# Kernel tuning notes

Measured on AMD Instinct MI355X. Metric: run time of the kernel, lower is better.

Reference implementation:

```python
import jax, jax.numpy as jnp
import numpy as np
import math

B, S, HID = 2, 2048, 1024
NH = 16
HD = HID // NH  # 64
CHUNK = 128  # min(128, S) from the module


def setup_inputs() -> dict:
    key = jax.random.key(0)
    ks = jax.random.split(key, 8)
    scale = 1.0 / math.sqrt(HID)
    return {
        "hidden_states": jax.random.normal(ks[0], (B, S, HID), jnp.float32),
        "attention_mask": jnp.zeros((B, S, S), jnp.float32),
        "Wq": jax.random.normal(ks[1], (HID, HID), jnp.float32) * scale,
        "bq": jnp.zeros((HID,), jnp.float32),
        "Wk": jax.random.normal(ks[2], (HID, HID), jnp.float32) * scale,
        "bk": jnp.zeros((HID,), jnp.float32),
        "Wv": jax.random.normal(ks[3], (HID, HID), jnp.float32) * scale,
        "bv": jnp.zeros((HID,), jnp.float32),
        "head_weights": jnp.ones((NH,), jnp.float32),
    }


def _split_heads(x):
    # [B,S,HID] -> [B,NH,S,HD]
    b, s, _ = x.shape
    return x.reshape(b, s, NH, HD).transpose(0, 2, 1, 3)


def reference(hidden_states, attention_mask, Wq, bq, Wk, bk, Wv, bv, head_weights):
    # nn.Linear: y = x @ W.T + b
    q = _split_heads(hidden_states @ Wq.T + bq)  # [B,NH,S,HD]
    k = _split_heads(hidden_states @ Wk.T + bk)
    v = _split_heads(hidden_states @ Wv.T + bv)

    scores = jnp.einsum("bhqd,bhkd->bhqk", q, k) / math.sqrt(HD)
    scores = scores + attention_mask[:, None, :, :]  # additive mask broadcast over heads
    probs = jax.nn.softmax(scores, axis=-1)
    # dropout p=0.0 -> identity; post-softmax head-weight scaling (head_pruning)
    probs = probs * head_weights[None, :, None, None]
    ctx = jnp.einsum("bhqk,bhkd->bhqd", probs, v)  # [B,NH,S,HD]
    context_layer = ctx.transpose(0, 2, 1, 3).reshape(B, S, HID)

    # module returns the probs of the LAST query chunk of the python loop
    last_start = ((S + CHUNK - 1) // CHUNK - 1) * CHUNK
    output_attention_probs = probs[:, :, last_start:S, :]  # [B,NH,128,S]
    return context_layer, output_attention_probs
```

## Files before the change

### kernel.cpp

```cpp
#include <hip/hip_runtime.h>

typedef unsigned short u16;
typedef __attribute__((ext_vector_type(8))) short bf16x8;
typedef __attribute__((ext_vector_type(4))) float f32x4;

#define B_   2
#define S_   2048
#define HID_ 1024
#define NH_  16
#define HD_  64
#define SCALE_ 0.125f

__device__ __forceinline__ u16 f2bf(float f) {
    union { float f; unsigned int i; } v; v.f = f;
    unsigned int r = v.i + 0x7fffu + ((v.i >> 16) & 1u);
    return (u16)(r >> 16);
}
__device__ __forceinline__ bf16x8 ld8(const u16* p) {
    return *reinterpret_cast<const bf16x8*>(p);
}
__device__ __forceinline__ void gll16(const u16* g, const u16* l) {
    __builtin_amdgcn_global_load_lds(
        (const __attribute__((address_space(1))) unsigned int*)g,
        (__attribute__((address_space(3))) unsigned int*)l, 16, 0, 0);
}

__global__ __launch_bounds__(256) void convert_bf16(
    const float* __restrict__ X, const float* __restrict__ W0,
    const float* __restrict__ W1, const float* __restrict__ W2,
    u16* __restrict__ Xb, u16* __restrict__ Wb)
{
    const size_t s = (size_t)blockIdx.x * 256 + threadIdx.x;
    const float* src; u16* dst; size_t off;
    if (s < 524288) { src = X; dst = Xb; off = s * 8; }
    else {
        const size_t t = s - 524288;
        const int w = (int)(t >> 17);
        off = (t & 131071) * 8;
        src = w == 0 ? W0 : w == 1 ? W1 : W2;
        dst = Wb + (size_t)w * 1048576;
    }
    f32x4 a = *(const f32x4*)(src + off);
    f32x4 b = *(const f32x4*)(src + off + 4);
    bf16x8 r;
    #pragma unroll
    for (int e = 0; e < 4; e++) { r[e] = (short)f2bf(a[e]); r[4 + e] = (short)f2bf(b[e]); }
    *(bf16x8*)(dst + off) = r;
}

__global__ __launch_bounds__(256) void mask_scan(
    const unsigned* __restrict__ m, unsigned* __restrict__ flag)
{
    const size_t i = ((size_t)blockIdx.x * 256 + threadIdx.x) * 8;
    const uint4* p = (const uint4*)(m + i);
    uint4 a = p[0], b = p[1];
    const unsigned M = 0x7fffffffu;
    unsigned v = (a.x & M) | (a.y & M) | (a.z & M) | (a.w & M)
               | (b.x & M) | (b.y & M) | (b.z & M) | (b.w & M);
    if (v) atomicOr(flag, 1u);
}

#define BK_ 32

__global__ __launch_bounds__(256) void qkv_mfma(
    const u16* __restrict__ Xb, const u16* __restrict__ Wb,
    const float* __restrict__ bq, const float* __restrict__ bk,
    const float* __restrict__ bv,
    u16* __restrict__ Q, u16* __restrict__ K, u16* __restrict__ V)
{
    __shared__ __align__(16) u16 As[128 * BK_];
    __shared__ __align__(16) u16 Bs[128 * BK_];

    const int tid  = threadIdx.x;
    const int wave = tid >> 6;
    const int lane = tid & 63;
    const int l16  = lane & 15;
    const int quad = lane >> 4;
    const int wr   = wave >> 1, wc = wave & 1;

    const int i0 = blockIdx.x * 128;
    const int j0 = blockIdx.y * 128;

    const int grow = (wave * 64 + lane) >> 2;
    const int gcol = (lane & 3) * 8;
    const u16* ldsA0 = As + wave * 512;
    const u16* ldsA1 = As + 2048 + wave * 512;
    const u16* ldsB0 = Bs + wave * 512;
    const u16* ldsB1 = Bs + 2048 + wave * 512;

    f32x4 acc[4][4] = {};

    for (int k0 = 0; k0 < HID_; k0 += BK_) {
        __syncthreads();
        gll16(Xb + (size_t)(i0 + grow) * HID_ + k0 + gcol, ldsA0);
        gll16(Xb + (size_t)(i0 + 64 + grow) * HID_ + k0 + gcol, ldsA1);
        gll16(Wb + (size_t)(j0 + grow) * HID_ + k0 + gcol, ldsB0);
        gll16(Wb + (size_t)(j0 + 64 + grow) * HID_ + k0 + gcol, ldsB1);
        __syncthreads();

        bf16x8 af[4], bfr[4];
        #pragma unroll
        for (int mt = 0; mt < 4; mt++)
            af[mt] = ld8(&As[(wr * 64 + mt * 16 + l16) * BK_ + quad * 8]);
        #pragma unroll
        for (int nt = 0; nt < 4; nt++)
            bfr[nt] = ld8(&Bs[(wc * 64 + nt * 16 + l16) * BK_ + quad * 8]);
        #pragma unroll
        for (int mt = 0; mt < 4; mt++)
            #pragma unroll
            for (int nt = 0; nt < 4; nt++)
                acc[mt][nt] = __builtin_amdgcn_mfma_f32_16x16x32_bf16(af[mt], bfr[nt], acc[mt][nt], 0, 0, 0);
    }

    const int which = j0 >> 10;
    const float* bias = which == 0 ? bq : which == 1 ? bk : bv;
    u16* Y            = which == 0 ? Q  : which == 1 ? K  : V;

    u16* bb = (wave < 2) ? (As + wave * 2048) : (Bs + (wave - 2) * 2048);

    #pragma unroll
    for (int p = 0; p < 2; p++) {
        __syncthreads();
        #pragma unroll
        for (int t2 = 0; t2 < 2; t2++) {
            const int nt = 2 * p + t2;
            const int j  = j0 + wc * 64 + nt * 16 + l16;
            const int jj = j & 1023;
            const float bv_ = bias[jj];
            #pragma unroll
            for (int mt = 0; mt < 4; mt++)
                #pragma unroll
                for (int r = 0; r < 4; r++) {
                    const int row = mt * 16 + quad * 4 + r;
                    const int col = t2 * 16 + l16;
                    const u16 val = f2bf(acc[mt][nt][r] + bv_);
                    if (which == 2)
                        bb[col * 64 + (row ^ ((col & 7) << 3))] = val;
                    else
                        bb[row * 32 + (col ^ ((row & 0xC) << 1))] = val;
                }
        }
        __syncthreads();
        #pragma unroll
        for (int k = 0; k < 4; k++) {
            const int c = lane + 64 * k;
            if (which == 2) {
                const int col  = c >> 3;
                const int row0 = (c & 7) * 8;
                bf16x8 v = ld8(&bb[col * 64 + (row0 ^ ((col & 7) << 3))]);
                const int j  = j0 + wc * 64 + p * 32 + col;
                const int jj = j & 1023;
                const int h = jj >> 6, d = jj & 63;
                const int i = i0 + wr * 64 + row0;
                const int b = i >> 11, s = i & (S_ - 1);
                *(bf16x8*)&Y[((size_t)(b * NH_ + h) * HD_ + d) * S_ + s] = v;
            } else {
                const int row  = c >> 2;
                const int col0 = (c & 3) * 8;
                bf16x8 v = ld8(&bb[row * 32 + (col0 ^ ((row & 0xC) << 1))]);
                const int j  = j0 + wc * 64 + p * 32 + col0;
                const int jj = j & 1023;
                const int h = jj >> 6, d = jj & 63;
                const int i = i0 + wr * 64 + row;
                const int b = i >> 11, s = i & (S_ - 1);
                *(bf16x8*)&Y[(((size_t)(b * NH_ + h) * S_ + s) * HD_) + d] = v;
            }
        }
    }
}

__global__ __launch_bounds__(256) void attn(
    const u16* __restrict__ Q, const u16* __restrict__ K, const u16* __restrict__ Vt,
    const float* __restrict__ mask, const float* __restrict__ hw,
    const unsigned* __restrict__ mflag,
    float* __restrict__ ctx, float* __restrict__ probs_out, float* __restrict__ ml)
{
    __shared__ __align__(16) u16 Ks[2][64 * 64];
    __shared__ __align__(16) u16 Vs[2][64 * 64];
    __shared__ __align__(16) u16 Pl[4][16 * 64];

    const int usemask = (mflag[0] != 0);

    const int tid  = threadIdx.x;
    const int wave = tid >> 6;
    const int lane = tid & 63;
    const int l16  = lane & 15;
    const int quad = lane >> 4;
    const int x7   = l16 & 7;

    const int lin = blockIdx.x + 32 * (blockIdx.y + 16 * blockIdx.z);
    const int xcd = lin & 7, jj = lin >> 3;
    const int qb  = jj & 31;
    const int hb  = xcd * 4 + (jj >> 5);
    const int h   = hb & 15, b = hb >> 4;
    const int bh  = b * NH_ + h;

    const u16* Qh  = Q  + (size_t)bh * S_ * HD_;
    const u16* Kh  = K  + (size_t)bh * S_ * HD_;
    const u16* Vth = Vt + (size_t)bh * HD_ * S_;
    const float* Mb = mask + (size_t)b * S_ * S_;

    const int q0 = qb * 64 + wave * 16;

    bf16x8 qf0 = ld8(Qh + (size_t)(q0 + l16) * HD_ + quad * 8);
    bf16x8 qf1 = ld8(Qh + (size_t)(q0 + l16) * HD_ + 32 + quad * 8);

    f32x4 oacc[4] = {};
    float l_part[4] = {0.f, 0.f, 0.f, 0.f};

    const int srow = tid >> 3;
    const int sch  = tid & 7;
    const int ssw  = (sch ^ (srow & 7)) * 8;
    const int sL   = srow * 64 + ssw;

    {
        bf16x8 k0 = ld8(Kh + (size_t)srow * HD_ + sch * 8);
        bf16x8 k1 = ld8(Kh + (size_t)(srow + 32) * HD_ + sch * 8);
        bf16x8 v0 = ld8(Vth + (size_t)srow * S_ + sch * 8);
        bf16x8 v1 = ld8(Vth + (size_t)(srow + 32) * S_ + sch * 8);
        *(bf16x8*)&Ks[0][sL] = k0; *(bf16x8*)&Ks[0][sL + 2048] = k1;
        *(bf16x8*)&Vs[0][sL] = v0; *(bf16x8*)&Vs[0][sL + 2048] = v1;
    }
    __syncthreads();

    for (int t = 0; t < 32; ++t) {
        const int cur = t & 1;
        const int kt  = t * 64;
        const u16* Kb = Ks[cur];
        const u16* Vb = Vs[cur];

        bf16x8 kr0, kr1, vr0, vr1;
        if (t < 31) {
            const u16* Kg = Kh + (size_t)(kt + 64) * HD_;
            kr0 = ld8(Kg + (size_t)srow * HD_ + sch * 8);
            kr1 = ld8(Kg + (size_t)(srow + 32) * HD_ + sch * 8);
            vr0 = ld8(Vth + (size_t)srow * S_ + kt + 64 + sch * 8);
            vr1 = ld8(Vth + (size_t)(srow + 32) * S_ + kt + 64 + sch * 8);
        }

        f32x4 sacc[4] = {};
        #pragma unroll
        for (int nb = 0; nb < 4; nb++) {
            const int base = (nb * 16 + l16) * 64;
            bf16x8 k0 = ld8(&Kb[base + ((quad ^ x7) * 8)]);
            bf16x8 k1 = ld8(&Kb[base + (((quad + 4) ^ x7) * 8)]);
            sacc[nb] = __builtin_amdgcn_mfma_f32_16x16x32_bf16(qf0, k0, sacc[nb], 0, 0, 0);
            sacc[nb] = __builtin_amdgcn_mfma_f32_16x16x32_bf16(qf1, k1, sacc[nb], 0, 0, 0);
        }
        float sc[4][4];
        if (usemask) {
            #pragma unroll
            for (int nb = 0; nb < 4; nb++)
                #pragma unroll
                for (int r = 0; r < 4; r++) {
                    const int qrow = q0 + quad * 4 + r;
                    const int key  = kt + nb * 16 + l16;
                    sc[nb][r] = sacc[nb][r] * SCALE_ + Mb[(size_t)qrow * S_ + key];
                }
        } else {
            #pragma unroll
            for (int nb = 0; nb < 4; nb++)
                #pragma unroll
                for (int r = 0; r < 4; r++) sc[nb][r] = sacc[nb][r] * SCALE_;
        }

        if (qb >= 30) {
            #pragma unroll
            for (int nb = 0; nb < 4; nb++)
                #pragma unroll
                for (int r = 0; r < 4; r++) {
                    const int qrow = q0 + quad * 4 + r;
                    const int key  = kt + nb * 16 + l16;
                    probs_out[((size_t)bh * 128 + (qrow - 1920)) * S_ + key] = sc[nb][r];
                }
        }

        u16 pb[4][4];
        #pragma unroll
        for (int nb = 0; nb < 4; nb++)
            #pragma unroll
            for (int r = 0; r < 4; r++) {
                float p = __expf(fminf(sc[nb][r], 80.f));
                l_part[r] += p;
                pb[nb][r] = f2bf(p);
            }

        #pragma unroll
        for (int nb = 0; nb < 4; nb++)
            #pragma unroll
            for (int r = 0; r < 4; r++) {
                const int row = quad * 4 + r;
                const int boff = (nb * 32 + l16 * 2) ^ ((row & 7) << 4);
                *(u16*)((char*)&Pl[wave][0] + row * 128 + boff) = pb[nb][r];
            }

        #pragma unroll
        for (int kb = 0; kb < 2; kb++) {
            const int c = kb * 4 + quad;
            bf16x8 pf = ld8(&Pl[wave][l16 * 64 + ((c ^ x7) * 8)]);
            #pragma unroll
            for (int db = 0; db < 4; db++) {
                bf16x8 vf = ld8(&Vb[(db * 16 + l16) * 64 + ((c ^ x7) * 8)]);
                oacc[db] = __builtin_amdgcn_mfma_f32_16x16x32_bf16(pf, vf, oacc[db], 0, 0, 0);
            }
        }

        if (t < 31) {
            u16* Kd = Ks[cur ^ 1]; u16* Vd = Vs[cur ^ 1];
            *(bf16x8*)&Kd[sL] = kr0; *(bf16x8*)&Kd[sL + 2048] = kr1;
            *(bf16x8*)&Vd[sL] = vr0; *(bf16x8*)&Vd[sL + 2048] = vr1;
        }
        __syncthreads();
    }

    float l_i[4];
    #pragma unroll
    for (int r = 0; r < 4; r++) {
        float s = l_part[r];
        #pragma unroll
        for (int off = 1; off < 16; off <<= 1) s += __shfl_xor(s, off);
        l_i[r] = s;
    }

    const float hwf = hw[h];
    float invl[4];
    #pragma unroll
    for (int r = 0; r < 4; r++) invl[r] = hwf / l_i[r];

    #pragma unroll
    for (int db = 0; db < 4; db++)
        #pragma unroll
        for (int r = 0; r < 4; r++) {
            const int qrow = q0 + quad * 4 + r;
            ctx[((size_t)(b * S_ + qrow)) * HID_ + h * HD_ + db * 16 + l16] =
                oacc[db][r] * invl[r];
        }

    if (qb >= 30 && l16 == 0) {
        #pragma unroll
        for (int r = 0; r < 4; r++) {
            const int qrow = q0 + quad * 4 + r;
            ml[bh * 128 + (qrow - 1920)] = l_i[r];
        }
    }
}

__global__ __launch_bounds__(256) void probs_finish(
    float* __restrict__ probs, const float* __restrict__ ml,
    const float* __restrict__ hw)
{
    const size_t i = ((size_t)blockIdx.x * 256 + threadIdx.x) * 4;
    const int row = (int)(i >> 11);
    const int h   = (row >> 7) & 15;
    const float s = hw[h] / ml[row];
    float4 v = *(float4*)(probs + i);
    v.x = __expf(fminf(v.x, 80.f)) * s;
    v.y = __expf(fminf(v.y, 80.f)) * s;
    v.z = __expf(fminf(v.z, 80.f)) * s;
    v.w = __expf(fminf(v.w, 80.f)) * s;
    *(float4*)(probs + i) = v;
}

extern "C" void kernel_launch(void* const* d_in, const int* in_sizes, int n_in,
                              void* d_out, int out_size, void* d_ws, size_t ws_size,
                              hipStream_t stream)
{
    const void* X = 0; const void* mask = 0; const void* hw = 0;
    const void* Wm[3] = {0, 0, 0}; const void* bm[3] = {0, 0, 0};
    int wi = 0, bi = 0;
    for (int i = 0; i < n_in; i++) {
        switch (in_sizes[i]) {
            case 4194304: X = d_in[i]; break;
            case 8388608: mask = d_in[i]; break;
            case 1048576: if (wi < 3) Wm[wi++] = d_in[i]; break;
            case 1024:    if (bi < 3) bm[bi++] = d_in[i]; break;
            case 16:      hw = d_in[i]; break;
            default: break;
        }
    }
    if (!X || !mask || wi != 3 || bi != 3 || !hw) {
        X = d_in[0]; mask = d_in[1];
        Wm[0] = d_in[2]; bm[0] = d_in[3];
        Wm[1] = d_in[4]; bm[1] = d_in[5];
        Wm[2] = d_in[6]; bm[2] = d_in[7];
        hw = d_in[8];
    }

    u16* Q  = (u16*)d_ws;
    u16* Kw = Q + 4194304ull;
    u16* Vw = Kw + 4194304ull;
    u16* Xb = Vw + 4194304ull;
    u16* Wb = Xb + 4194304ull;
    unsigned* flag = (unsigned*)(Wb + 3145728ull);
    float* ml = (float*)(flag + 64);

    float* ctx   = (float*)d_out;
    float* probs = ctx + (size_t)B_ * S_ * HID_;

    hipMemsetAsync(flag, 0, 4, stream);
    mask_scan<<<4096, 256, 0, stream>>>((const unsigned*)mask, flag);
    convert_bf16<<<3584, 256, 0, stream>>>(
        (const float*)X, (const float*)Wm[0], (const float*)Wm[1], (const float*)Wm[2],
        Xb, Wb);

    qkv_mfma<<<dim3(32, 24), dim3(256), 0, stream>>>(
        Xb, Wb, (const float*)bm[0], (const float*)bm[1], (const float*)bm[2],
        Q, Kw, Vw);

    attn<<<dim3(32, 16, 2), dim3(256), 0, stream>>>(
        Q, Kw, Vw, (const float*)mask, (const float*)hw, flag, ctx, probs, ml);

    probs_finish<<<8192, 256, 0, stream>>>(probs, ml, (const float*)hw);
}
```

Before: 256.6 us.

## Double-buffer QKV GEMM, fuse probs normalization into attention, add setprio and packed bf16 cvt

The QKV GEMM now double-buffers its LDS tiles and prefetches the next K slice while the current one feeds the MFMAs, leaving one barrier per iteration. In the attention kernel, exp is computed once and unnormalized probabilities are written for the last query chunk. Those rows are then rescaled in place at the end of the kernel, which removes the separate probs_finish launch and the ml buffer. It also adds s_setprio around the MFMA sections and uses packed v_cvt_pk_bf16_f32 conversion for P. The in-kernel rescale rereads each row from global memory after stores made by other lanes in the same wave, so correctness depends on that visibility holding.

```diff
diff --git a/kernel.cpp b/kernel.cpp
--- a/kernel.cpp
+++ b/kernel.cpp
@@ -18,6 +18,11 @@
 }
 __device__ __forceinline__ bf16x8 ld8(const u16* p) {
     return *reinterpret_cast<const bf16x8*>(p);
+}
+__device__ __forceinline__ unsigned cvtpk(float lo, float hi) {
+    unsigned r;
+    asm("v_cvt_pk_bf16_f32 %0, %1, %2" : "=v"(r) : "v"(lo), "v"(hi));
+    return r;
 }
 __device__ __forceinline__ void gll16(const u16* g, const u16* l) {
     __builtin_amdgcn_global_load_lds(
@@ -68,8 +73,8 @@
     const float* __restrict__ bv,
     u16* __restrict__ Q, u16* __restrict__ K, u16* __restrict__ V)
 {
-    __shared__ __align__(16) u16 As[128 * BK_];
-    __shared__ __align__(16) u16 Bs[128 * BK_];
+    __shared__ __align__(16) u16 As[2][128 * BK_];
+    __shared__ __align__(16) u16 Bs[2][128 * BK_];
 
     const int tid  = threadIdx.x;
     const int wave = tid >> 6;
@@ -81,42 +86,46 @@
     const int i0 = blockIdx.x * 128;
     const int j0 = blockIdx.y * 128;
 
-    const int grow = (wave * 64 + lane) >> 2;
+    const int grow = tid >> 2;
     const int gcol = (lane & 3) * 8;
-    const u16* ldsA0 = As + wave * 512;
-    const u16* ldsA1 = As + 2048 + wave * 512;
-    const u16* ldsB0 = Bs + wave * 512;
-    const u16* ldsB1 = Bs + 2048 + wave * 512;
 
     f32x4 acc[4][4] = {};
 
-    for (int k0 = 0; k0 < HID_; k0 += BK_) {
-        __syncthreads();
-        gll16(Xb + (size_t)(i0 + grow) * HID_ + k0 + gcol, ldsA0);
-        gll16(Xb + (size_t)(i0 + 64 + grow) * HID_ + k0 + gcol, ldsA1);
-        gll16(Wb + (size_t)(j0 + grow) * HID_ + k0 + gcol, ldsB0);
-        gll16(Wb + (size_t)(j0 + 64 + grow) * HID_ + k0 + gcol, ldsB1);
-        __syncthreads();
+    auto stage = [&](int bf, int k0) {
+        gll16(Xb + (size_t)(i0 + grow) * HID_ + k0 + gcol, &As[bf][wave * 512]);
+        gll16(Xb + (size_t)(i0 + 64 + grow) * HID_ + k0 + gcol, &As[bf][2048 + wave * 512]);
+        gll16(Wb + (size_t)(j0 + grow) * HID_ + k0 + gcol, &Bs[bf][wave * 512]);
+        gll16(Wb + (size_t)(j0 + 64 + grow) * HID_ + k0 + gcol, &Bs[bf][2048 + wave * 512]);
+    };
+
+    stage(0, 0);
+    __syncthreads();
+
+    for (int t = 0; t < 32; t++) {
+        const int cur = t & 1;
+        if (t < 31) stage(cur ^ 1, (t + 1) * BK_);
 
         bf16x8 af[4], bfr[4];
         #pragma unroll
         for (int mt = 0; mt < 4; mt++)
-            af[mt] = ld8(&As[(wr * 64 + mt * 16 + l16) * BK_ + quad * 8]);
+            af[mt] = ld8(&As[cur][(wr * 64 + mt * 16 + l16) * BK_ + quad * 8]);
         #pragma unroll
         for (int nt = 0; nt < 4; nt++)
-            bfr[nt] = ld8(&Bs[(wc * 64 + nt * 16 + l16) * BK_ + quad * 8]);
+            bfr[nt] = ld8(&Bs[cur][(wc * 64 + nt * 16 + l16) * BK_ + quad * 8]);
         #pragma unroll
         for (int mt = 0; mt < 4; mt++)
             #pragma unroll
             for (int nt = 0; nt < 4; nt++)
                 acc[mt][nt] = __builtin_amdgcn_mfma_f32_16x16x32_bf16(af[mt], bfr[nt], acc[mt][nt], 0, 0, 0);
+
+        __syncthreads();
     }
 
     const int which = j0 >> 10;
     const float* bias = which == 0 ? bq : which == 1 ? bk : bv;
     u16* Y            = which == 0 ? Q  : which == 1 ? K  : V;
 
-    u16* bb = (wave < 2) ? (As + wave * 2048) : (Bs + (wave - 2) * 2048);
+    u16* bb = (wave < 2) ? &As[0][wave * 2048] : &Bs[0][(wave - 2) * 2048];
 
     #pragma unroll
     for (int p = 0; p < 2; p++) {
@@ -173,7 +182,7 @@
     const u16* __restrict__ Q, const u16* __restrict__ K, const u16* __restrict__ Vt,
     const float* __restrict__ mask, const float* __restrict__ hw,
     const unsigned* __restrict__ mflag,
-    float* __restrict__ ctx, float* __restrict__ probs_out, float* __restrict__ ml)
+    float* __restrict__ ctx, float* __restrict__ probs_out)
 {
     __shared__ __align__(16) u16 Ks[2][64 * 64];
     __shared__ __align__(16) u16 Vs[2][64 * 64];
@@ -239,6 +248,7 @@
         }
 
         f32x4 sacc[4] = {};
+        __builtin_amdgcn_s_setprio(1);
         #pragma unroll
         for (int nb = 0; nb < 4; nb++) {
             const int base = (nb * 16 + l16) * 64;
@@ -247,7 +257,9 @@
             sacc[nb] = __builtin_amdgcn_mfma_f32_16x16x32_bf16(qf0, k0, sacc[nb], 0, 0, 0);
             sacc[nb] = __builtin_amdgcn_mfma_f32_16x16x32_bf16(qf1, k1, sacc[nb], 0, 0, 0);
         }
-        float sc[4][4];
+        __builtin_amdgcn_s_setprio(0);
+
+        float p[4][4];
         if (usemask) {
             #pragma unroll
             for (int nb = 0; nb < 4; nb++)
@@ -255,13 +267,18 @@
                 for (int r = 0; r < 4; r++) {
                     const int qrow = q0 + quad * 4 + r;
                     const int key  = kt + nb * 16 + l16;
-                    sc[nb][r] = sacc[nb][r] * SCALE_ + Mb[(size_t)qrow * S_ + key];
+                    float s = sacc[nb][r] * SCALE_ + Mb[(size_t)qrow * S_ + key];
+                    p[nb][r] = __expf(fminf(s, 80.f));
+                    l_part[r] += p[nb][r];
                 }
         } else {
             #pragma unroll
             for (int nb = 0; nb < 4; nb++)
                 #pragma unroll
-                for (int r = 0; r < 4; r++) sc[nb][r] = sacc[nb][r] * SCALE_;
+                for (int r = 0; r < 4; r++) {
+                    p[nb][r] = __expf(fminf(sacc[nb][r] * SCALE_, 80.f));
+                    l_part[r] += p[nb][r];
+                }
         }
 
         if (qb >= 30) {
@@ -271,29 +288,26 @@
                 for (int r = 0; r < 4; r++) {
                     const int qrow = q0 + quad * 4 + r;
                     const int key  = kt + nb * 16 + l16;
-                    probs_out[((size_t)bh * 128 + (qrow - 1920)) * S_ + key] = sc[nb][r];
+                    probs_out[((size_t)bh * 128 + (qrow - 1920)) * S_ + key] = p[nb][r];
                 }
         }
 
-        u16 pb[4][4];
-        #pragma unroll
-        for (int nb = 0; nb < 4; nb++)
-            #pragma unroll
-            for (int r = 0; r < 4; r++) {
-                float p = __expf(fminf(sc[nb][r], 80.f));
-                l_part[r] += p;
-                pb[nb][r] = f2bf(p);
+        {
+            char* pbase = (char*)&Pl[wave][0];
+            const int r0 = quad * 4;
+            #pragma unroll
+            for (int nb = 0; nb < 4; nb++) {
+                const unsigned w01 = cvtpk(p[nb][0], p[nb][1]);
+                const unsigned w23 = cvtpk(p[nb][2], p[nb][3]);
+                const int c0 = nb * 32 + l16 * 2;
+                *(u16*)(pbase + (r0 + 0) * 128 + (c0 ^ (((r0 + 0) & 7) << 4))) = (u16)w01;
+                *(u16*)(pbase + (r0 + 1) * 128 + (c0 ^ (((r0 + 1) & 7) << 4))) = (u16)(w01 >> 16);
+                *(u16*)(pbase + (r0 + 2) * 128 + (c0 ^ (((r0 + 2) & 7) << 4))) = (u16)w23;
+                *(u16*)(pbase + (r0 + 3) * 128 + (c0 ^ (((r0 + 3) & 7) << 4))) = (u16)(w23 >> 16);
             }
-
-        #pragma unroll
-        for (int nb = 0; nb < 4; nb++)
-            #pragma unroll
-            for (int r = 0; r < 4; r++) {
-                const int row = quad * 4 + r;
-                const int boff = (nb * 32 + l16 * 2) ^ ((row & 7) << 4);
-                *(u16*)((char*)&Pl[wave][0] + row * 128 + boff) = pb[nb][r];
-            }
-
+        }
+
+        __builtin_amdgcn_s_setprio(1);
         #pragma unroll
         for (int kb = 0; kb < 2; kb++) {
             const int c = kb * 4 + quad;
@@ -304,6 +318,7 @@
                 oacc[db] = __builtin_amdgcn_mfma_f32_16x16x32_bf16(pf, vf, oacc[db], 0, 0, 0);
             }
         }
+        __builtin_amdgcn_s_setprio(0);
 
         if (t < 31) {
             u16* Kd = Ks[cur ^ 1]; u16* Vd = Vs[cur ^ 1];
@@ -336,29 +351,20 @@
                 oacc[db][r] * invl[r];
         }
 
-    if (qb >= 30 && l16 == 0) {
+    if (qb >= 30) {
+        __threadfence();
         #pragma unroll
         for (int r = 0; r < 4; r++) {
-            const int qrow = q0 + quad * 4 + r;
-            ml[bh * 128 + (qrow - 1920)] = l_i[r];
-        }
-    }
-}
-
-__global__ __launch_bounds__(256) void probs_finish(
-    float* __restrict__ probs, const float* __restrict__ ml,
-    const float* __restrict__ hw)
-{
-    const size_t i = ((size_t)blockIdx.x * 256 + threadIdx.x) * 4;
-    const int row = (int)(i >> 11);
-    const int h   = (row >> 7) & 15;
-    const float s = hw[h] / ml[row];
-    float4 v = *(float4*)(probs + i);
-    v.x = __expf(fminf(v.x, 80.f)) * s;
-    v.y = __expf(fminf(v.y, 80.f)) * s;
-    v.z = __expf(fminf(v.z, 80.f)) * s;
-    v.w = __expf(fminf(v.w, 80.f)) * s;
-    *(float4*)(probs + i) = v;
+            const int prow = q0 - 1920 + quad * 4 + r;
+            float4* P4 = (float4*)(probs_out + ((size_t)bh * 128 + prow) * S_);
+            const float sc = invl[r];
+            for (int i = l16; i < 512; i += 16) {
+                float4 v = P4[i];
+                v.x *= sc; v.y *= sc; v.z *= sc; v.w *= sc;
+                P4[i] = v;
+            }
+        }
+    }
 }
 
 extern "C" void kernel_launch(void* const* d_in, const int* in_sizes, int n_in,
@@ -392,7 +398,6 @@
     u16* Xb = Vw + 4194304ull;
     u16* Wb = Xb + 4194304ull;
     unsigned* flag = (unsigned*)(Wb + 3145728ull);
-    float* ml = (float*)(flag + 64);
 
     float* ctx   = (float*)d_out;
     float* probs = ctx + (size_t)B_ * S_ * HID_;
@@ -408,7 +413,5 @@
         Q, Kw, Vw);
 
     attn<<<dim3(32, 16, 2), dim3(256), 0, stream>>>(
-        Q, Kw, Vw, (const float*)mask, (const float*)hw, flag, ctx, probs, ml);
-
-    probs_finish<<<8192, 256, 0, stream>>>(probs, ml, (const float*)hw);
-}
+        Q, Kw, Vw, (const float*)mask, (const float*)hw, flag, ctx, probs);
+}
```

Result: slower. 283.0 us (+10.3%).
